# Optimization experiments

Hardware: AMD Instinct MI355X
Metric: run time of the kernel (lower is better)

## Reference

```python
import jax, jax.numpy as jnp
import numpy as np
import math

B, S, E = 4, 4096, 1024
NUM_HEADS = 16
D = E // NUM_HEADS  # attention_size = 64


def setup_inputs() -> dict:
    key = jax.random.key(0)
    ks = jax.random.split(key, 7)
    queries = jax.random.normal(ks[0], (B, S, E), dtype=jnp.float32)
    keys = jax.random.normal(ks[1], (B, S, E), dtype=jnp.float32)
    values = jax.random.normal(ks[2], (B, S, E), dtype=jnp.float32)
    mask = jax.random.randint(ks[3], (B, S, S), 0, 2).astype(bool)
    # nn.Linear(E, D, bias=False): weight [D, E], y = x @ W^T
    lim = 1.0 / math.sqrt(E)
    W_q = jax.random.uniform(ks[4], (D, E), jnp.float32, -lim, lim)
    W_k = jax.random.uniform(ks[5], (D, E), jnp.float32, -lim, lim)
    W_v = jax.random.uniform(ks[6], (D, E), jnp.float32, -lim, lim)
    return {"queries": queries, "keys": keys, "values": values, "mask": mask,
            "W_q": W_q, "W_k": W_k, "W_v": W_v}


def reference(queries, keys, values, mask, W_q, W_k, W_v):
    Q = jnp.einsum('bse,de->bsd', queries, W_q)  # [B,S,D]
    K = jnp.einsum('bse,de->bsd', keys, W_k)
    V = jnp.einsum('bse,de->bsd', values, W_v)
    norm = math.sqrt(D)
    scores = jnp.einsum('bqd,bkd->bqk', Q, K) / norm  # [B,S,S]
    scores = jnp.where(mask, jnp.float32(-1e20), scores)
    attn = jax.nn.softmax(scores, axis=2)
    return jnp.einsum('bqk,bkd->bqd', attn, V)  # [B,S,D]
```

## Files before the change

kernel.cpp:

```cpp
#include <hip/hip_runtime.h>
#include <hip/hip_bf16.h>
#include <math.h>

#define NB 4
#define NS 4096
#define NE 1024
#define ND 64

typedef short bf16x8 __attribute__((ext_vector_type(8)));
typedef float f32x4  __attribute__((ext_vector_type(4)));

static __device__ inline unsigned short f2bf(float f) {
    __hip_bfloat16 h = __float2bfloat16(f);
    return *reinterpret_cast<unsigned short*>(&h);
}

__global__ void detect_mask(const unsigned int* __restrict__ mw, int* __restrict__ flag) {
    __shared__ int found;
    if (threadIdx.x == 0) found = 0;
    __syncthreads();
    int f = 0;
    for (int i = threadIdx.x; i < 4096; i += 256)
        if (mw[i] > 1u) f = 1;
    if (f) atomicOr(&found, 1);
    __syncthreads();
    if (threadIdx.x == 0) *flag = found;
}

__global__ void prep_w(const float* __restrict__ Wq, const float* __restrict__ Wk,
                       const float* __restrict__ Wv, unsigned short* __restrict__ Wb) {
    const int z = blockIdx.x;
    const float* W = (z == 0) ? Wq : (z == 1) ? Wk : Wv;
    unsigned short* o = Wb + (size_t)z * (ND * NE);
    const float scale = (z == 0) ? 0.125f : 1.0f;
    int i0 = blockIdx.y * 2048 + threadIdx.x * 8;
    float4 a = *(const float4*)&W[i0];
    float4 b = *(const float4*)&W[i0 + 4];
    ushort4 u0 = { f2bf(a.x * scale), f2bf(a.y * scale), f2bf(a.z * scale), f2bf(a.w * scale) };
    ushort4 u1 = { f2bf(b.x * scale), f2bf(b.y * scale), f2bf(b.z * scale), f2bf(b.w * scale) };
    *(ushort4*)&o[i0]     = u0;
    *(ushort4*)&o[i0 + 4] = u1;
}

__global__ __launch_bounds__(256) void proj_kernel(
    const float* __restrict__ Xq, const float* __restrict__ Xk, const float* __restrict__ Xv,
    const unsigned short* __restrict__ Wb,
    unsigned short* __restrict__ Qp, unsigned short* __restrict__ Kp,
    unsigned short* __restrict__ Vtp)
{
    const int z = blockIdx.y;
    const float* X = (z == 0) ? Xq : (z == 1) ? Xk : Xv;
    const unsigned short* W = Wb + (size_t)z * (ND * NE);

    const int t    = threadIdx.x;
    const int wv   = t >> 6;
    const int lane = t & 63;
    const int quad = lane >> 4;
    const int l16  = lane & 15;
    const int m0   = blockIdx.x * 64 + wv * 16;

    const float* Xrow = X + (size_t)(m0 + l16) * NE + quad * 8;

    f32x4 acc[4] = {};

    #pragma unroll 4
    for (int e0 = 0; e0 < NE; e0 += 32) {
        float4 xa = *(const float4*)&Xrow[e0];
        float4 xb = *(const float4*)&Xrow[e0 + 4];
        bf16x8 a;
        a[0] = (short)f2bf(xa.x); a[1] = (short)f2bf(xa.y);
        a[2] = (short)f2bf(xa.z); a[3] = (short)f2bf(xa.w);
        a[4] = (short)f2bf(xb.x); a[5] = (short)f2bf(xb.y);
        a[6] = (short)f2bf(xb.z); a[7] = (short)f2bf(xb.w);
        #pragma unroll
        for (int nt = 0; nt < 4; ++nt) {
            bf16x8 b = *(const bf16x8*)&W[(size_t)(nt * 16 + l16) * NE + e0 + quad * 8];
            acc[nt] = __builtin_amdgcn_mfma_f32_16x16x32_bf16(a, b, acc[nt], 0, 0, 0);
        }
    }

    #pragma unroll
    for (int nt = 0; nt < 4; ++nt)
        #pragma unroll
        for (int r = 0; r < 4; ++r) {
            int m   = m0 + quad * 4 + r;
            int col = nt * 16 + l16;
            unsigned short u = f2bf(acc[nt][r]);
            if (z == 0)      Qp[(size_t)m * ND + col] = u;
            else if (z == 1) Kp[(size_t)m * ND + col] = u;
            else             Vtp[((size_t)(m >> 12) * ND + col) * NS + (m & 4095)] = u;
        }
}

__global__ __launch_bounds__(256) void attn_kernel(
    const unsigned short* __restrict__ Qp, const unsigned short* __restrict__ Kp,
    const unsigned short* __restrict__ Vtp,
    const void* __restrict__ maskp, const int* __restrict__ flagp,
    float* __restrict__ out)
{
    __shared__ short Ss[4][2][16][72];
    __shared__ float Op[4][16][68];
    __shared__ float Lp[4][16];

    const int t    = threadIdx.x;
    const int wv   = t >> 6;
    const int lane = t & 63;
    const int quad = lane >> 4;
    const int l16  = lane & 15;
    const int b    = blockIdx.y;
    const int q0   = blockIdx.x * 16;
    const int koff = wv * 1024;

    const bool m_u8 = (*flagp != 0);
    const unsigned char* m8  = (const unsigned char*)maskp;
    const int*           m32 = (const int*)maskp;

    const unsigned short* Qrow = Qp + ((size_t)b * NS + q0 + l16) * ND;
    const bf16x8 qf0 = *(const bf16x8*)&Qrow[quad * 8];
    const bf16x8 qf1 = *(const bf16x8*)&Qrow[32 + quad * 8];

    const unsigned short* Kbase = Kp  + ((size_t)b * NS) * ND;
    const unsigned short* Vbase = Vtp + (size_t)b * ND * NS;

    float l_lane[4] = {};
    f32x4 Oacc[4] = {};

    #pragma unroll 2
    for (int it = 0; it < 16; ++it) {
        const int k0 = koff + it * 64;
        const int pb = it & 1;

        int mv[16];
        #pragma unroll
        for (int r = 0; r < 4; ++r) {
            size_t mrow = ((size_t)b * NS + (q0 + quad * 4 + r)) * (size_t)NS + k0;
            if (m_u8) {
                #pragma unroll
                for (int kt = 0; kt < 4; ++kt)
                    mv[kt * 4 + r] = (int)m8[mrow + kt * 16 + l16];
            } else {
                #pragma unroll
                for (int kt = 0; kt < 4; ++kt)
                    mv[kt * 4 + r] = m32[mrow + kt * 16 + l16];
            }
        }

        f32x4 sc[4] = {};
        #pragma unroll
        for (int kt = 0; kt < 4; ++kt) {
            const unsigned short* Krow = Kbase + (size_t)(k0 + kt * 16 + l16) * ND;
            bf16x8 kf0 = *(const bf16x8*)&Krow[quad * 8];
            bf16x8 kf1 = *(const bf16x8*)&Krow[32 + quad * 8];
            sc[kt] = __builtin_amdgcn_mfma_f32_16x16x32_bf16(qf0, kf0, sc[kt], 0, 0, 0);
            sc[kt] = __builtin_amdgcn_mfma_f32_16x16x32_bf16(qf1, kf1, sc[kt], 0, 0, 0);
        }

        #pragma unroll
        for (int kt = 0; kt < 4; ++kt)
            #pragma unroll
            for (int r = 0; r < 4; ++r) {
                float p = mv[kt * 4 + r] ? 0.0f : __expf(sc[kt][r]);
                l_lane[r] += p;
                Ss[wv][pb][quad * 4 + r][kt * 16 + l16] = (short)f2bf(p);
            }

        __syncthreads();

        bf16x8 a0 = *(const bf16x8*)&Ss[wv][pb][l16][quad * 8];
        bf16x8 a1 = *(const bf16x8*)&Ss[wv][pb][l16][32 + quad * 8];

        #pragma unroll
        for (int nt = 0; nt < 4; ++nt) {
            const unsigned short* Vrow = Vbase + (size_t)(nt * 16 + l16) * NS + k0;
            bf16x8 vf0 = *(const bf16x8*)&Vrow[quad * 8];
            bf16x8 vf1 = *(const bf16x8*)&Vrow[32 + quad * 8];
            Oacc[nt] = __builtin_amdgcn_mfma_f32_16x16x32_bf16(a0, vf0, Oacc[nt], 0, 0, 0);
            Oacc[nt] = __builtin_amdgcn_mfma_f32_16x16x32_bf16(a1, vf1, Oacc[nt], 0, 0, 0);
        }
    }

    #pragma unroll
    for (int r = 0; r < 4; ++r) {
        #pragma unroll
        for (int off = 1; off < 16; off <<= 1)
            l_lane[r] += __shfl_xor(l_lane[r], off);
    }

    #pragma unroll
    for (int nt = 0; nt < 4; ++nt)
        #pragma unroll
        for (int r = 0; r < 4; ++r)
            Op[wv][quad * 4 + r][nt * 16 + l16] = Oacc[nt][r];
    if (l16 == 0) {
        #pragma unroll
        for (int r = 0; r < 4; ++r)
            Lp[wv][quad * 4 + r] = l_lane[r];
    }
    __syncthreads();

    {
        int q  = t >> 4;
        int d4 = (t & 15) * 4;
        f32x4 s = {};
        #pragma unroll
        for (int w = 0; w < 4; ++w)
            s += *(const f32x4*)&Op[w][q][d4];
        float l = Lp[0][q] + Lp[1][q] + Lp[2][q] + Lp[3][q];
        float inv = 1.0f / l;
        float4 o = { s[0] * inv, s[1] * inv, s[2] * inv, s[3] * inv };
        *(float4*)&out[((size_t)b * NS + q0 + q) * ND + d4] = o;
    }
}

extern "C" void kernel_launch(void* const* d_in, const int* in_sizes, int n_in,
                              void* d_out, int out_size, void* d_ws, size_t ws_size,
                              hipStream_t stream) {
    const float* queries = (const float*)d_in[0];
    const float* keys    = (const float*)d_in[1];
    const float* values  = (const float*)d_in[2];
    const void*  mask    = d_in[3];
    const float* Wq      = (const float*)d_in[4];
    const float* Wk      = (const float*)d_in[5];
    const float* Wv      = (const float*)d_in[6];
    float* out = (float*)d_out;

    char* ws = (char*)d_ws;
    int* flag = (int*)ws;
    unsigned short* Wb = (unsigned short*)(ws + 256);
    size_t wb = (size_t)3 * ND * NE * sizeof(unsigned short);
    size_t pb = (size_t)NB * NS * ND * sizeof(unsigned short);
    unsigned short* Qp  = (unsigned short*)(ws + 256 + wb);
    unsigned short* Kp  = (unsigned short*)(ws + 256 + wb + pb);
    unsigned short* Vtp = (unsigned short*)(ws + 256 + wb + 2 * pb);

    hipLaunchKernelGGL(detect_mask, dim3(1), dim3(256), 0, stream,
                       (const unsigned int*)mask, flag);
    hipLaunchKernelGGL(prep_w, dim3(3, 32), dim3(256), 0, stream, Wq, Wk, Wv, Wb);
    hipLaunchKernelGGL(proj_kernel, dim3((NB * NS) / 64, 3), dim3(256), 0, stream,
                       queries, keys, values, Wb, Qp, Kp, Vtp);
    hipLaunchKernelGGL(attn_kernel, dim3(NS / 16, NB), dim3(256), 0, stream,
                       Qp, Kp, Vtp, mask, flag, out);
}
```

Baseline: 581.8 us.

## Coalesce mask loads via LDS, shrink attention smem, merge prep kernels

Several changes at once. The attention kernel now loads each mask tile with one coalesced 16-byte load per lane and stages it in LDS instead of issuing scattered per-element byte loads. Shared memory is shrunk by overlaying buffers, dropping the double-buffered score tile, and reducing the partial outputs with LDS atomics, with a launch bound asking for 5 blocks per CU to raise occupancy. The projection kernel stages the X tile through LDS with coalesced loads, and the mask-detect and weight-prep kernels are merged into one launch. The costs are an extra barrier per iteration and atomic contention in the epilogue.

```diff
diff --git a/kernel.cpp b/kernel.cpp
--- a/kernel.cpp
+++ b/kernel.cpp
@@ -15,25 +15,27 @@
     return *reinterpret_cast<unsigned short*>(&h);
 }
 
-__global__ void detect_mask(const unsigned int* __restrict__ mw, int* __restrict__ flag) {
-    __shared__ int found;
-    if (threadIdx.x == 0) found = 0;
-    __syncthreads();
-    int f = 0;
-    for (int i = threadIdx.x; i < 4096; i += 256)
-        if (mw[i] > 1u) f = 1;
-    if (f) atomicOr(&found, 1);
-    __syncthreads();
-    if (threadIdx.x == 0) *flag = found;
-}
-
-__global__ void prep_w(const float* __restrict__ Wq, const float* __restrict__ Wk,
-                       const float* __restrict__ Wv, unsigned short* __restrict__ Wb) {
-    const int z = blockIdx.x;
+__global__ void prep_kernel(const float* __restrict__ Wq, const float* __restrict__ Wk,
+                            const float* __restrict__ Wv, unsigned short* __restrict__ Wb,
+                            const unsigned int* __restrict__ mw, int* __restrict__ flag) {
+    if (blockIdx.x == 96) {
+        __shared__ int found;
+        if (threadIdx.x == 0) found = 0;
+        __syncthreads();
+        int f = 0;
+        for (int i = threadIdx.x; i < 4096; i += 256)
+            if (mw[i] > 1u) f = 1;
+        if (f) atomicOr(&found, 1);
+        __syncthreads();
+        if (threadIdx.x == 0) *flag = found;
+        return;
+    }
+    const int z = blockIdx.x >> 5;
+    const int chunk = blockIdx.x & 31;
     const float* W = (z == 0) ? Wq : (z == 1) ? Wk : Wv;
     unsigned short* o = Wb + (size_t)z * (ND * NE);
     const float scale = (z == 0) ? 0.125f : 1.0f;
-    int i0 = blockIdx.y * 2048 + threadIdx.x * 8;
+    int i0 = chunk * 2048 + threadIdx.x * 8;
     float4 a = *(const float4*)&W[i0];
     float4 b = *(const float4*)&W[i0 + 4];
     ushort4 u0 = { f2bf(a.x * scale), f2bf(a.y * scale), f2bf(a.z * scale), f2bf(a.w * scale) };
@@ -48,6 +50,8 @@
     unsigned short* __restrict__ Qp, unsigned short* __restrict__ Kp,
     unsigned short* __restrict__ Vtp)
 {
+    __shared__ short Xs[64][72];
+
     const int z = blockIdx.y;
     const float* X = (z == 0) ? Xq : (z == 1) ? Xk : Xv;
     const unsigned short* W = Wb + (size_t)z * (ND * NE);
@@ -57,25 +61,31 @@
     const int lane = t & 63;
     const int quad = lane >> 4;
     const int l16  = lane & 15;
-    const int m0   = blockIdx.x * 64 + wv * 16;
-
-    const float* Xrow = X + (size_t)(m0 + l16) * NE + quad * 8;
+    const int m0   = blockIdx.x * 64;
 
     f32x4 acc[4] = {};
 
-    #pragma unroll 4
-    for (int e0 = 0; e0 < NE; e0 += 32) {
-        float4 xa = *(const float4*)&Xrow[e0];
-        float4 xb = *(const float4*)&Xrow[e0 + 4];
-        bf16x8 a;
-        a[0] = (short)f2bf(xa.x); a[1] = (short)f2bf(xa.y);
-        a[2] = (short)f2bf(xa.z); a[3] = (short)f2bf(xa.w);
-        a[4] = (short)f2bf(xb.x); a[5] = (short)f2bf(xb.y);
-        a[6] = (short)f2bf(xb.z); a[7] = (short)f2bf(xb.w);
+    for (int e0 = 0; e0 < NE; e0 += 64) {
+        __syncthreads();
+        #pragma unroll
+        for (int i = 0; i < 4; ++i) {
+            int idx = t + i * 256;
+            int row = idx >> 4, c4 = (idx & 15) * 4;
+            float4 v = *(const float4*)&X[(size_t)(m0 + row) * NE + e0 + c4];
+            short4 s = { (short)f2bf(v.x), (short)f2bf(v.y),
+                         (short)f2bf(v.z), (short)f2bf(v.w) };
+            *(short4*)&Xs[row][c4] = s;
+        }
+        __syncthreads();
+        bf16x8 a0 = *(const bf16x8*)&Xs[wv * 16 + l16][quad * 8];
+        bf16x8 a1 = *(const bf16x8*)&Xs[wv * 16 + l16][32 + quad * 8];
         #pragma unroll
         for (int nt = 0; nt < 4; ++nt) {
-            bf16x8 b = *(const bf16x8*)&W[(size_t)(nt * 16 + l16) * NE + e0 + quad * 8];
-            acc[nt] = __builtin_amdgcn_mfma_f32_16x16x32_bf16(a, b, acc[nt], 0, 0, 0);
+            const unsigned short* Wr = W + (size_t)(nt * 16 + l16) * NE + e0 + quad * 8;
+            bf16x8 b0 = *(const bf16x8*)&Wr[0];
+            bf16x8 b1 = *(const bf16x8*)&Wr[32];
+            acc[nt] = __builtin_amdgcn_mfma_f32_16x16x32_bf16(a0, b0, acc[nt], 0, 0, 0);
+            acc[nt] = __builtin_amdgcn_mfma_f32_16x16x32_bf16(a1, b1, acc[nt], 0, 0, 0);
         }
     }
 
@@ -83,7 +93,7 @@
     for (int nt = 0; nt < 4; ++nt)
         #pragma unroll
         for (int r = 0; r < 4; ++r) {
-            int m   = m0 + quad * 4 + r;
+            int m   = m0 + wv * 16 + quad * 4 + r;
             int col = nt * 16 + l16;
             unsigned short u = f2bf(acc[nt][r]);
             if (z == 0)      Qp[(size_t)m * ND + col] = u;
@@ -92,15 +102,21 @@
         }
 }
 
-__global__ __launch_bounds__(256) void attn_kernel(
+#define SS(w,r,c) Ss[(((w) * 16 + (r)) * 72) + (c)]
+#define MS(w,r,c) Ms[(((w) * 16 + (r)) * 80) + (c)]
+#define OP(r,c)   Op[((r) * 68) + (c)]
+__global__ __launch_bounds__(256, 5) void attn_kernel(
     const unsigned short* __restrict__ Qp, const unsigned short* __restrict__ Kp,
     const unsigned short* __restrict__ Vtp,
     const void* __restrict__ maskp, const int* __restrict__ flagp,
     float* __restrict__ out)
 {
-    __shared__ short Ss[4][2][16][72];
-    __shared__ float Op[4][16][68];
-    __shared__ float Lp[4][16];
+    __shared__ uint4 smem4[904];
+    char* smem = (char*)smem4;
+    short* Ss = (short*)smem;
+    unsigned char* Ms = (unsigned char*)(smem + 9216);
+    float* Op = (float*)smem;
+    float* Lr = (float*)(smem + 14336);
 
     const int t    = threadIdx.x;
     const int wv   = t >> 6;
@@ -122,27 +138,26 @@
     const unsigned short* Kbase = Kp  + ((size_t)b * NS) * ND;
     const unsigned short* Vbase = Vtp + (size_t)b * ND * NS;
 
+    const int mrow = lane >> 2;
+    const int mc16 = (lane & 3) * 16;
+
     float l_lane[4] = {};
     f32x4 Oacc[4] = {};
 
-    #pragma unroll 2
     for (int it = 0; it < 16; ++it) {
         const int k0 = koff + it * 64;
-        const int pb = it & 1;
-
-        int mv[16];
-        #pragma unroll
-        for (int r = 0; r < 4; ++r) {
-            size_t mrow = ((size_t)b * NS + (q0 + quad * 4 + r)) * (size_t)NS + k0;
-            if (m_u8) {
-                #pragma unroll
-                for (int kt = 0; kt < 4; ++kt)
-                    mv[kt * 4 + r] = (int)m8[mrow + kt * 16 + l16];
-            } else {
-                #pragma unroll
-                for (int kt = 0; kt < 4; ++kt)
-                    mv[kt * 4 + r] = m32[mrow + kt * 16 + l16];
-            }
+
+        if (m_u8) {
+            uint4 mval = *(const uint4*)&m8[((size_t)b * NS + q0 + mrow) * NS + k0 + mc16];
+            *(uint4*)&MS(wv, mrow, mc16) = mval;
+        } else {
+            const int* mp = &m32[((size_t)b * NS + q0 + mrow) * NS + k0 + mc16];
+            unsigned int w[4] = {0, 0, 0, 0};
+            #pragma unroll
+            for (int j = 0; j < 16; ++j)
+                w[j >> 2] |= (mp[j] ? 1u : 0u) << ((j & 3) * 8);
+            uint4 pk = { w[0], w[1], w[2], w[3] };
+            *(uint4*)&MS(wv, mrow, mc16) = pk;
         }
 
         f32x4 sc[4] = {};
@@ -155,20 +170,22 @@
             sc[kt] = __builtin_amdgcn_mfma_f32_16x16x32_bf16(qf1, kf1, sc[kt], 0, 0, 0);
         }
 
+        __syncthreads();
+
         #pragma unroll
         for (int kt = 0; kt < 4; ++kt)
             #pragma unroll
             for (int r = 0; r < 4; ++r) {
-                float p = mv[kt * 4 + r] ? 0.0f : __expf(sc[kt][r]);
+                unsigned char mb = MS(wv, quad * 4 + r, kt * 16 + l16);
+                float p = mb ? 0.0f : __expf(sc[kt][r]);
                 l_lane[r] += p;
-                Ss[wv][pb][quad * 4 + r][kt * 16 + l16] = (short)f2bf(p);
+                SS(wv, quad * 4 + r, kt * 16 + l16) = (short)f2bf(p);
             }
 
         __syncthreads();
 
-        bf16x8 a0 = *(const bf16x8*)&Ss[wv][pb][l16][quad * 8];
-        bf16x8 a1 = *(const bf16x8*)&Ss[wv][pb][l16][32 + quad * 8];
-
+        bf16x8 a0 = *(const bf16x8*)&SS(wv, l16, quad * 8);
+        bf16x8 a1 = *(const bf16x8*)&SS(wv, l16, 32 + quad * 8);
         #pragma unroll
         for (int nt = 0; nt < 4; ++nt) {
             const unsigned short* Vrow = Vbase + (size_t)(nt * 16 + l16) * NS + k0;
@@ -186,27 +203,27 @@
             l_lane[r] += __shfl_xor(l_lane[r], off);
     }
 
+    __syncthreads();
+    for (int i = t; i < 16 * 68; i += 256) Op[i] = 0.0f;
+    if (t < 16) Lr[t] = 0.0f;
+    __syncthreads();
     #pragma unroll
     for (int nt = 0; nt < 4; ++nt)
         #pragma unroll
         for (int r = 0; r < 4; ++r)
-            Op[wv][quad * 4 + r][nt * 16 + l16] = Oacc[nt][r];
+            atomicAdd(&OP(quad * 4 + r, nt * 16 + l16), Oacc[nt][r]);
     if (l16 == 0) {
         #pragma unroll
         for (int r = 0; r < 4; ++r)
-            Lp[wv][quad * 4 + r] = l_lane[r];
+            atomicAdd(&Lr[quad * 4 + r], l_lane[r]);
     }
     __syncthreads();
 
     {
         int q  = t >> 4;
         int d4 = (t & 15) * 4;
-        f32x4 s = {};
-        #pragma unroll
-        for (int w = 0; w < 4; ++w)
-            s += *(const f32x4*)&Op[w][q][d4];
-        float l = Lp[0][q] + Lp[1][q] + Lp[2][q] + Lp[3][q];
-        float inv = 1.0f / l;
+        f32x4 s = *(const f32x4*)&OP(q, d4);
+        float inv = 1.0f / Lr[q];
         float4 o = { s[0] * inv, s[1] * inv, s[2] * inv, s[3] * inv };
         *(float4*)&out[((size_t)b * NS + q0 + q) * ND + d4] = o;
     }
@@ -233,9 +250,8 @@
     unsigned short* Kp  = (unsigned short*)(ws + 256 + wb + pb);
     unsigned short* Vtp = (unsigned short*)(ws + 256 + wb + 2 * pb);
 
-    hipLaunchKernelGGL(detect_mask, dim3(1), dim3(256), 0, stream,
-                       (const unsigned int*)mask, flag);
-    hipLaunchKernelGGL(prep_w, dim3(3, 32), dim3(256), 0, stream, Wq, Wk, Wv, Wb);
+    hipLaunchKernelGGL(prep_kernel, dim3(97), dim3(256), 0, stream,
+                       Wq, Wk, Wv, Wb, (const unsigned int*)mask, flag);
     hipLaunchKernelGGL(proj_kernel, dim3((NB * NS) / 64, 3), dim3(256), 0, stream,
                        queries, keys, values, Wb, Qp, Kp, Vtp);
     hipLaunchKernelGGL(attn_kernel, dim3(NS / 16, NB), dim3(256), 0, stream,
```

New measurement: 603.7 us. +3.8%, slower.
